# Performance work log

Measured on AMD Instinct MI355X. Metric: run time of the kernel, lower is better.

Reference implementation:

```python
import jax, jax.numpy as jnp
import numpy as np

B, S, D, H, HID = 64, 1024, 128, 4, 512
HD = D // H  # head dim = 32
EPS = 1e-5


def layer_norm(x, gamma, beta):
    mu = jnp.mean(x, axis=-1, keepdims=True)
    var = jnp.mean(jnp.square(x - mu), axis=-1, keepdims=True)
    return (x - mu) * jax.lax.rsqrt(var + EPS) * gamma + beta


def setup_inputs() -> dict:
    key = jax.random.key(0)
    ks = jax.random.split(key, 16)
    w = lambda k, shp: (jax.random.normal(k, shp, dtype=jnp.float32) * 0.02)
    return {
        "seq": jax.random.normal(ks[0], (B, S, D), dtype=jnp.float32),
        "mask": jnp.ones((B, S, 1), dtype=jnp.float32),
        "Wq": w(ks[1], (D, D)), "bq": jnp.zeros((D,), jnp.float32),
        "Wk": w(ks[2], (D, D)), "bk": jnp.zeros((D,), jnp.float32),
        "Wv": w(ks[3], (D, D)), "bv": jnp.zeros((D,), jnp.float32),
        "g1": jnp.ones((D,), jnp.float32), "be1": jnp.zeros((D,), jnp.float32),
        "g2": jnp.ones((D,), jnp.float32), "be2": jnp.zeros((D,), jnp.float32),
        "W1": w(ks[4], (D, HID)), "bm1": jnp.zeros((HID,), jnp.float32),
        "W2": w(ks[5], (HID, D)), "bm2": jnp.zeros((D,), jnp.float32),
    }


def reference(seq, mask, Wq, bq, Wk, bk, Wv, bv, g1, be1, g2, be2, W1, bm1, W2, bm2):
    # pre-norm queries; keys/values come from the RAW seq (SASRec quirk)
    q_in = layer_norm(seq, g1, be1)           # [B,S,D]
    keys = seq

    Q = (q_in @ Wq + bq).reshape(B, S, H, HD)
    K = (keys @ Wk + bk).reshape(B, S, H, HD)
    V = (keys @ Wv + bv).reshape(B, S, H, HD)

    scores = jnp.einsum("bqhd,bkhd->bhqk", Q, K) / jnp.sqrt(jnp.float32(HD))

    # key padding mask from sign of abs-sum over feature dim
    key_mask = jnp.sign(jnp.sum(jnp.abs(keys), axis=-1))      # [B,S]
    scores = jnp.where(key_mask[:, None, None, :] == 0, -jnp.inf, scores)

    # causal mask
    causal = jnp.tril(jnp.ones((S, S), dtype=bool))
    scores = jnp.where(causal[None, None], scores, -jnp.inf)

    w = jax.nn.softmax(scores, axis=-1)
    w = jnp.nan_to_num(w, nan=0.0, posinf=0.0, neginf=0.0)

    # query padding mask (on the NORMALIZED queries)
    query_mask = jnp.sign(jnp.sum(jnp.abs(q_in), axis=-1))    # [B,S]
    w = w * query_mask[:, None, :, None]
    attentions = w                                            # [B,H,S,S]

    attn_out = jnp.einsum("bhqk,bkhd->bqhd", w, V).reshape(B, S, D)

    x = attn_out + q_in
    x = layer_norm(x, g2, be2)
    h = jax.nn.relu(x @ W1 + bm1)
    y = h @ W2 + bm2 + x
    y = y * mask
    return y, attentions
```

## Files before the change

### kernel.cpp

```cpp
#include <hip/hip_runtime.h>
#include <cstddef>
#include <cstdint>

#define BB 64
#define SS 1024
#define DDIM 128
#define NH 4
#define HDIM 32
#define HIDD 512
#define EPSF 1e-5f
#define SCALEF 0.17677669529663687f

typedef __attribute__((ext_vector_type(8))) short short8;
typedef __attribute__((ext_vector_type(4))) short short4_t;
typedef __attribute__((ext_vector_type(4))) float f32x4;
typedef unsigned short ushort_t;

__device__ __forceinline__ unsigned short f2bf(float f) {
  unsigned u = __builtin_bit_cast(unsigned, f);
  unsigned r = (u + 0x7FFFu + ((u >> 16) & 1u)) >> 16;
  return (unsigned short)r;
}
__device__ __forceinline__ float bf2f(ushort_t h) {
  unsigned u = ((unsigned)h) << 16;
  return __builtin_bit_cast(float, u);
}

__global__ __launch_bounds__(256) void k_cvtw(
    const float* __restrict__ Wq, const float* __restrict__ Wk,
    const float* __restrict__ Wv, const float* __restrict__ W1,
    const float* __restrict__ W2,
    ushort_t* __restrict__ WqT, ushort_t* __restrict__ WkT,
    ushort_t* __restrict__ WvT, ushort_t* __restrict__ W1T,
    ushort_t* __restrict__ W2T) {
  __shared__ float tile[32][33];
  const int bid = blockIdx.x;
  const float* src; ushort_t* dst; int K, N, t0;
  if (bid < 16)       { src = Wq; dst = WqT; K = 128; N = 128; t0 = bid; }
  else if (bid < 32)  { src = Wk; dst = WkT; K = 128; N = 128; t0 = bid - 16; }
  else if (bid < 48)  { src = Wv; dst = WvT; K = 128; N = 128; t0 = bid - 32; }
  else if (bid < 112) { src = W1; dst = W1T; K = 128; N = 512; t0 = bid - 48; }
  else                { src = W2; dst = W2T; K = 512; N = 128; t0 = bid - 112; }
  const int ntile = N >> 5;
  const int k0 = (t0 / ntile) * 32, n0 = (t0 % ntile) * 32;
  const int t = threadIdx.x;
  const int r = t >> 3, c = (t & 7) * 4;
  float4 v = *(const float4*)(src + (size_t)(k0 + r) * N + n0 + c);
  tile[r][c] = v.x; tile[r][c + 1] = v.y; tile[r][c + 2] = v.z; tile[r][c + 3] = v.w;
  __syncthreads();
  ushort4 o;
  o.x = f2bf(tile[c + 0][r]); o.y = f2bf(tile[c + 1][r]);
  o.z = f2bf(tile[c + 2][r]); o.w = f2bf(tile[c + 3][r]);
  *(ushort4*)(dst + (size_t)(n0 + r) * K + k0 + c) = o;
}

__global__ __launch_bounds__(128) void k_ln1(const float* __restrict__ seq,
    const float* __restrict__ g1, const float* __restrict__ be1,
    ushort_t* __restrict__ q_in16, ushort_t* __restrict__ seq16,
    float* __restrict__ qmask, float* __restrict__ kmask) {
  int row = blockIdx.x, t = threadIdx.x;
  float v = seq[(size_t)row * DDIM + t];
  float s = v, a = fabsf(v);
  #pragma unroll
  for (int o = 32; o; o >>= 1) { s += __shfl_down(s, o); a += __shfl_down(a, o); }
  __shared__ float sm[4], sm2[2], sm3[2];
  if ((t & 63) == 0) { sm[t >> 6] = s; sm[2 + (t >> 6)] = a; }
  __syncthreads();
  float mean = (sm[0] + sm[1]) * (1.f / DDIM);
  float asum = sm[2] + sm[3];
  float d = v - mean;
  float sq = d * d;
  #pragma unroll
  for (int o = 32; o; o >>= 1) sq += __shfl_down(sq, o);
  if ((t & 63) == 0) sm2[t >> 6] = sq;
  __syncthreads();
  float var = (sm2[0] + sm2[1]) * (1.f / DDIM);
  float qv = d * rsqrtf(var + EPSF) * g1[t] + be1[t];
  q_in16[(size_t)row * DDIM + t] = f2bf(qv);
  seq16[(size_t)row * DDIM + t] = f2bf(v);
  float aq = fabsf(qv);
  #pragma unroll
  for (int o = 32; o; o >>= 1) aq += __shfl_down(aq, o);
  if ((t & 63) == 0) sm3[t >> 6] = aq;
  __syncthreads();
  if (t == 0) {
    kmask[row] = asum > 0.f ? 1.f : 0.f;
    qmask[row] = (sm3[0] + sm3[1]) > 0.f ? 1.f : 0.f;
  }
}

__global__ __launch_bounds__(256) void k_qkv_mfma(
    const ushort_t* __restrict__ q_in16, const ushort_t* __restrict__ seq16,
    const ushort_t* __restrict__ WqT, const ushort_t* __restrict__ WkT,
    const ushort_t* __restrict__ WvT,
    const float* __restrict__ bq, const float* __restrict__ bk,
    const float* __restrict__ bv,
    ushort_t* __restrict__ Qo, ushort_t* __restrict__ Ko,
    ushort_t* __restrict__ Vo) {
  const int m = blockIdx.y;
  const ushort_t* A = (m == 0) ? q_in16 : seq16;
  const ushort_t* WT = (m == 0) ? WqT : (m == 1 ? WkT : WvT);
  const float* bias = (m == 0) ? bq : (m == 1 ? bk : bv);
  ushort_t* O = (m == 0) ? Qo : (m == 1 ? Ko : Vo);
  const float sc = (m == 0) ? SCALEF : 1.0f;
  const int t = threadIdx.x, w = t >> 6, lane = t & 63;
  const int lr = lane & 15, lg = lane >> 4;
  const int row = blockIdx.x * 64 + w * 16;

  short8 a[4];
  #pragma unroll
  for (int s = 0; s < 4; ++s)
    a[s] = *(const short8*)(A + (size_t)(row + lr) * DDIM + s * 32 + lg * 8);

  #pragma unroll
  for (int nt = 0; nt < 8; ++nt) {
    f32x4 acc = {0.f, 0.f, 0.f, 0.f};
    #pragma unroll
    for (int s = 0; s < 4; ++s) {
      short8 b = *(const short8*)(WT + (size_t)(nt * 16 + lr) * DDIM + s * 32 + lg * 8);
      acc = __builtin_amdgcn_mfma_f32_16x16x32_bf16(b, a[s], acc, 0, 0, 0);
    }
    const int n0 = nt * 16 + lg * 4;
    const float4 bb4 = *(const float4*)(bias + n0);
    short4_t o4;
    o4[0] = (short)f2bf((acc[0] + bb4.x) * sc);
    o4[1] = (short)f2bf((acc[1] + bb4.y) * sc);
    o4[2] = (short)f2bf((acc[2] + bb4.z) * sc);
    o4[3] = (short)f2bf((acc[3] + bb4.w) * sc);
    *(short4_t*)(O + (size_t)(row + lr) * DDIM + n0) = o4;
  }
}

__global__ __launch_bounds__(256) void k_attn_mfma(
    const ushort_t* __restrict__ Q, const ushort_t* __restrict__ K,
    const ushort_t* __restrict__ V,
    const float* __restrict__ qmask, const float* __restrict__ kmask,
    float* __restrict__ attn, float* __restrict__ xo) {
  __shared__ __align__(16) ushort_t Ks[64 * 40];
  __shared__ __align__(16) ushort_t Vts[32 * 72];
  __shared__ __align__(16) ushort_t Wb[4][16 * 88];

  const int t = threadIdx.x;
  const int w = t >> 6, lane = t & 63, lr = lane & 15, lg = lane >> 4;
  const int qi = 15 - (int)blockIdx.x;
  const int q0 = qi << 6;
  const int h = blockIdx.y, b = blockIdx.z;
  const int kend = q0 + 64;
  const int nch = kend >> 6;

  const size_t bS = (size_t)b * SS;
  const ushort_t* Qh = Q + bS * DDIM + h * HDIM;
  const ushort_t* Kh = K + bS * DDIM + h * HDIM;
  const ushort_t* Vh = V + bS * DDIM + h * HDIM;
  float* attn_bh = attn + (size_t)(b * NH + h) * ((size_t)SS * SS);

  {
    const int cnt4 = (SS - kend) >> 2;
    for (int r = w; r < 64; r += 4) {
      float* rowp = attn_bh + (size_t)(q0 + r) * SS + kend;
      for (int c = lane; c < cnt4; c += 64)
        *(f32x4*)(rowp + (size_t)c * 4) = (f32x4){0.f, 0.f, 0.f, 0.f};
    }
  }

  const int qrow = q0 + w * 16 + lr;
  const short8 qf = *(const short8*)(Qh + (size_t)qrow * DDIM + lg * 8);

  const int skr = t >> 2, skc = (t & 3) * 8;

  float lsum = 0.f;
  short8 kreg = *(const short8*)(Kh + (size_t)skr * DDIM + skc);

  for (int c = 0; c < nch; ++c) {
    const int kc = c << 6;
    __syncthreads();
    *(short8*)(Ks + skr * 40 + skc) = kreg;
    if (c + 1 < nch)
      kreg = *(const short8*)(Kh + (size_t)(kc + 64 + skr) * DDIM + skc);
    __syncthreads();
    short8 kf[4];
    #pragma unroll
    for (int T = 0; T < 4; ++T)
      kf[T] = *(const short8*)(Ks + (T * 16 + lr) * 40 + lg * 8);
    f32x4 acc[4];
    #pragma unroll
    for (int T = 0; T < 4; ++T)
      acc[T] = __builtin_amdgcn_mfma_f32_16x16x32_bf16(kf[T], qf,
                                                       (f32x4){0.f, 0.f, 0.f, 0.f}, 0, 0, 0);
    #pragma unroll
    for (int T = 0; T < 4; ++T) {
      const int k0 = kc + T * 16 + lg * 4;
      const float4 km4 = *(const float4*)(kmask + bS + k0);
      #pragma unroll
      for (int r = 0; r < 4; ++r) {
        const float kmv = r == 0 ? km4.x : (r == 1 ? km4.y : (r == 2 ? km4.z : km4.w));
        const bool dead = (kmv == 0.f) || (k0 + r > qrow);
        lsum += dead ? 0.f : __expf(acc[T][r]);
      }
    }
  }
  float ssum = lsum;
  ssum += __shfl_xor(ssum, 16);
  ssum += __shfl_xor(ssum, 32);
  const float qm = qmask[bS + qrow];
  const float inv = (ssum > 0.f) ? qm / ssum : 0.f;

  ushort_t* myW = &Wb[w][0];
  f32x4 o0 = {0.f, 0.f, 0.f, 0.f}, o1 = {0.f, 0.f, 0.f, 0.f};

  short8 kreg2 = *(const short8*)(Kh + (size_t)skr * DDIM + skc);
  short8 vreg  = *(const short8*)(Vh + (size_t)lane * DDIM + w * 8);

  for (int c = 0; c < nch; ++c) {
    const int kc = c << 6;
    __syncthreads();
    *(short8*)(Ks + skr * 40 + skc) = kreg2;
    #pragma unroll
    for (int j = 0; j < 8; ++j) Vts[(w * 8 + j) * 72 + lane] = (ushort_t)vreg[j];
    if (c + 1 < nch) {
      kreg2 = *(const short8*)(Kh + (size_t)(kc + 64 + skr) * DDIM + skc);
      vreg  = *(const short8*)(Vh + (size_t)(kc + 64 + lane) * DDIM + w * 8);
    }
    __syncthreads();
    short8 kf[4];
    #pragma unroll
    for (int T = 0; T < 4; ++T)
      kf[T] = *(const short8*)(Ks + (T * 16 + lr) * 40 + lg * 8);
    f32x4 acc[4];
    #pragma unroll
    for (int T = 0; T < 4; ++T)
      acc[T] = __builtin_amdgcn_mfma_f32_16x16x32_bf16(kf[T], qf,
                                                       (f32x4){0.f, 0.f, 0.f, 0.f}, 0, 0, 0);
    #pragma unroll
    for (int T = 0; T < 4; ++T) {
      const int k0 = kc + T * 16 + lg * 4;
      const float4 km4 = *(const float4*)(kmask + bS + k0);
      f32x4 wv4;
      #pragma unroll
      for (int r = 0; r < 4; ++r) {
        const float kmv = r == 0 ? km4.x : (r == 1 ? km4.y : (r == 2 ? km4.z : km4.w));
        const bool dead = (kmv == 0.f) || (k0 + r > qrow);
        wv4[r] = dead ? 0.f : __expf(acc[T][r]) * inv;
      }
      *(f32x4*)(attn_bh + (size_t)qrow * SS + k0) = wv4;
      short4_t p4;
      p4[0] = (short)f2bf(wv4[0]); p4[1] = (short)f2bf(wv4[1]);
      p4[2] = (short)f2bf(wv4[2]); p4[3] = (short)f2bf(wv4[3]);
      *(short4_t*)(myW + lr * 88 + T * 16 + lg * 4) = p4;
    }
    const short8 af0 = *(const short8*)(myW + lr * 88 + lg * 8);
    const short8 af1 = *(const short8*)(myW + lr * 88 + 32 + lg * 8);
    const short8 vb00 = *(const short8*)(Vts + (size_t)(lr) * 72 + lg * 8);
    const short8 vb10 = *(const short8*)(Vts + (size_t)(lr) * 72 + 32 + lg * 8);
    const short8 vb01 = *(const short8*)(Vts + (size_t)(16 + lr) * 72 + lg * 8);
    const short8 vb11 = *(const short8*)(Vts + (size_t)(16 + lr) * 72 + 32 + lg * 8);
    o0 = __builtin_amdgcn_mfma_f32_16x16x32_bf16(vb00, af0, o0, 0, 0, 0);
    o0 = __builtin_amdgcn_mfma_f32_16x16x32_bf16(vb10, af1, o0, 0, 0, 0);
    o1 = __builtin_amdgcn_mfma_f32_16x16x32_bf16(vb01, af0, o1, 0, 0, 0);
    o1 = __builtin_amdgcn_mfma_f32_16x16x32_bf16(vb11, af1, o1, 0, 0, 0);
  }

  {
    float* op = xo + (bS + qrow) * DDIM + h * HDIM;
    *(f32x4*)(op + lg * 4) = o0;
    *(f32x4*)(op + 16 + lg * 4) = o1;
  }
}

__global__ __launch_bounds__(256) void k_mlp_fused(
    const float* __restrict__ xo, const ushort_t* __restrict__ q_in16,
    const float* __restrict__ g2, const float* __restrict__ be2,
    const ushort_t* __restrict__ W1T, const float* __restrict__ bm1,
    const ushort_t* __restrict__ W2T, const float* __restrict__ bm2,
    const float* __restrict__ mask, float* __restrict__ y) {
  __shared__ __align__(16) ushort_t xls[64 * 136];
  __shared__ __align__(16) ushort_t hs[4][16 * 140];
  const int t = threadIdx.x, w = t >> 6, lane = t & 63;
  const int lr = lane & 15, lg = lane >> 4;
  const int row0 = blockIdx.x * 64;

  {
    const int r = t >> 2, s = t & 3;
    const size_t base = (size_t)(row0 + r) * DDIM + s * 32;
    float v[32];
    float sum = 0.f, sq = 0.f;
    #pragma unroll
    for (int i = 0; i < 4; ++i) {
      const f32x4 x4a = *(const f32x4*)(xo + base + i * 8);
      const f32x4 x4b = *(const f32x4*)(xo + base + i * 8 + 4);
      const short8 q8 = *(const short8*)(q_in16 + base + i * 8);
      #pragma unroll
      for (int j = 0; j < 4; ++j) {
        v[i * 8 + j] = x4a[j] + bf2f((ushort_t)q8[j]);
        v[i * 8 + 4 + j] = x4b[j] + bf2f((ushort_t)q8[4 + j]);
      }
    }
    #pragma unroll
    for (int i = 0; i < 32; ++i) { sum += v[i]; sq += v[i] * v[i]; }
    sum += __shfl_xor(sum, 1); sum += __shfl_xor(sum, 2);
    sq  += __shfl_xor(sq, 1);  sq  += __shfl_xor(sq, 2);
    const float mean = sum * (1.f / DDIM);
    const float var = sq * (1.f / DDIM) - mean * mean;
    const float rsq = rsqrtf(var + EPSF);
    #pragma unroll
    for (int i = 0; i < 8; ++i) {
      const f32x4 g4 = *(const f32x4*)(g2 + s * 32 + i * 4);
      const f32x4 b4 = *(const f32x4*)(be2 + s * 32 + i * 4);
      short4_t o4;
      #pragma unroll
      for (int j = 0; j < 4; ++j)
        o4[j] = (short)f2bf((v[i * 4 + j] - mean) * rsq * g4[j] + b4[j]);
      *(short4_t*)(xls + r * 136 + s * 32 + i * 4) = o4;
    }
  }
  __syncthreads();

  ushort_t* myh = &hs[w][0];
  short8 xa[4];
  #pragma unroll
  for (int s = 0; s < 4; ++s)
    xa[s] = *(const short8*)(xls + (w * 16 + lr) * 136 + s * 32 + lg * 8);

  f32x4 yacc[8];
  #pragma unroll
  for (int i = 0; i < 8; ++i) yacc[i] = (f32x4){0.f, 0.f, 0.f, 0.f};

  for (int c = 0; c < 4; ++c) {
    #pragma unroll
    for (int nt = 0; nt < 8; ++nt) {
      f32x4 acc = {0.f, 0.f, 0.f, 0.f};
      #pragma unroll
      for (int s = 0; s < 4; ++s) {
        short8 b = *(const short8*)(W1T + (size_t)(c * 128 + nt * 16 + lr) * DDIM + s * 32 + lg * 8);
        acc = __builtin_amdgcn_mfma_f32_16x16x32_bf16(b, xa[s], acc, 0, 0, 0);
      }
      const int n0 = nt * 16 + lg * 4;
      const float4 bb4 = *(const float4*)(bm1 + c * 128 + n0);
      short4_t hp;
      hp[0] = (short)f2bf(fmaxf(acc[0] + bb4.x, 0.f));
      hp[1] = (short)f2bf(fmaxf(acc[1] + bb4.y, 0.f));
      hp[2] = (short)f2bf(fmaxf(acc[2] + bb4.z, 0.f));
      hp[3] = (short)f2bf(fmaxf(acc[3] + bb4.w, 0.f));
      *(short4_t*)(myh + lr * 140 + n0) = hp;
    }
    short8 a2[4];
    #pragma unroll
    for (int s = 0; s < 4; ++s)
      a2[s] = *(const short8*)(myh + lr * 140 + s * 32 + lg * 8);
    #pragma unroll
    for (int nt = 0; nt < 8; ++nt) {
      #pragma unroll
      for (int s = 0; s < 4; ++s) {
        short8 b = *(const short8*)(W2T + (size_t)(nt * 16 + lr) * HIDD + c * 128 + s * 32 + lg * 8);
        yacc[nt] = __builtin_amdgcn_mfma_f32_16x16x32_bf16(b, a2[s], yacc[nt], 0, 0, 0);
      }
    }
  }

  const int rr = row0 + w * 16 + lr;
  const float mk = mask[rr];
  #pragma unroll
  for (int nt = 0; nt < 8; ++nt) {
    const int n0 = nt * 16 + lg * 4;
    const float4 bb4 = *(const float4*)(bm2 + n0);
    const ushort4 xv = *(const ushort4*)(xls + (w * 16 + lr) * 136 + n0);
    f32x4 out;
    out[0] = (yacc[nt][0] + bb4.x + bf2f(xv.x)) * mk;
    out[1] = (yacc[nt][1] + bb4.y + bf2f(xv.y)) * mk;
    out[2] = (yacc[nt][2] + bb4.z + bf2f(xv.z)) * mk;
    out[3] = (yacc[nt][3] + bb4.w + bf2f(xv.w)) * mk;
    *(f32x4*)(y + (size_t)rr * DDIM + n0) = out;
  }
}

extern "C" void kernel_launch(void* const* d_in, const int* in_sizes, int n_in,
                              void* d_out, int out_size, void* d_ws, size_t ws_size,
                              hipStream_t stream) {
  const float* seq  = (const float*)d_in[0];
  const float* mask = (const float*)d_in[1];
  const float* Wq = (const float*)d_in[2];
  const float* bq = (const float*)d_in[3];
  const float* Wk = (const float*)d_in[4];
  const float* bk = (const float*)d_in[5];
  const float* Wv = (const float*)d_in[6];
  const float* bv = (const float*)d_in[7];
  const float* g1 = (const float*)d_in[8];
  const float* be1 = (const float*)d_in[9];
  const float* g2 = (const float*)d_in[10];
  const float* be2 = (const float*)d_in[11];
  const float* W1 = (const float*)d_in[12];
  const float* bm1 = (const float*)d_in[13];
  const float* W2 = (const float*)d_in[14];
  const float* bm2 = (const float*)d_in[15];

  float* ws   = (float*)d_ws;
  float* xb   = ws;
  float* qmk  = ws + 8388608;
  float* kmk  = ws + 8454144;
  ushort_t* sbase  = (ushort_t*)(ws + 8519680);
  ushort_t* Qb     = sbase;
  ushort_t* Kb     = sbase + 8388608;
  ushort_t* Vb     = sbase + 16777216;
  ushort_t* q_in16 = sbase + 25165824;
  ushort_t* seq16  = sbase + 33554432;
  ushort_t* WqT    = sbase + 41943040;
  ushort_t* WkT    = WqT + 16384;
  ushort_t* WvT    = WkT + 16384;
  ushort_t* W1T    = WvT + 16384;
  ushort_t* W2T    = W1T + 65536;

  float* y    = (float*)d_out;
  float* attn = y + 8388608;

  hipLaunchKernelGGL(k_cvtw, dim3(176), dim3(256), 0, stream,
                     Wq, Wk, Wv, W1, W2, WqT, WkT, WvT, W1T, W2T);
  hipLaunchKernelGGL(k_ln1, dim3(BB * SS), dim3(128), 0, stream,
                     seq, g1, be1, q_in16, seq16, qmk, kmk);
  hipLaunchKernelGGL(k_qkv_mfma, dim3(1024, 3), dim3(256), 0, stream,
                     q_in16, seq16, WqT, WkT, WvT, bq, bk, bv, Qb, Kb, Vb);
  hipLaunchKernelGGL(k_attn_mfma, dim3(16, NH, BB), dim3(256), 0, stream,
                     Qb, Kb, Vb, qmk, kmk, attn, xb);
  hipLaunchKernelGGL(k_mlp_fused, dim3(1024), dim3(256), 0, stream,
                     xb, q_in16, g2, be2, W1T, bm1, W2T, bm2, mask, y);
}
```

Baseline: 672.8 us.

## Double-buffer attention K/V smem, use exp2 softmax, fuse K/V projection, vectorize LN1

The attention kernel now double-buffers its K and V shared-memory tiles, so each chunk needs one barrier instead of two and the next tile's global load overlaps compute. Q is pre-scaled by log2(e) so the softmax can use exp2f, and the attention-matrix writes become nontemporal stores. The QKV kernel computes K and V together from a single load of seq, which drops one grid slice. LayerNorm1 now handles 8 rows per block with float4 loads and warp-only reductions. Together these target barrier stalls, redundant input reads and cache pollution from the large attention output.

```diff
diff --git a/kernel.cpp b/kernel.cpp
--- a/kernel.cpp
+++ b/kernel.cpp
@@ -10,6 +10,7 @@
 #define HIDD 512
 #define EPSF 1e-5f
 #define SCALEF 0.17677669529663687f
+#define LOG2E 1.4426950408889634f
 
 typedef __attribute__((ext_vector_type(8))) short short8;
 typedef __attribute__((ext_vector_type(4))) short short4_t;
@@ -54,38 +55,43 @@
   *(ushort4*)(dst + (size_t)(n0 + r) * K + k0 + c) = o;
 }
 
-__global__ __launch_bounds__(128) void k_ln1(const float* __restrict__ seq,
+__global__ __launch_bounds__(256) void k_ln1(const float* __restrict__ seq,
     const float* __restrict__ g1, const float* __restrict__ be1,
     ushort_t* __restrict__ q_in16, ushort_t* __restrict__ seq16,
     float* __restrict__ qmask, float* __restrict__ kmask) {
-  int row = blockIdx.x, t = threadIdx.x;
-  float v = seq[(size_t)row * DDIM + t];
-  float s = v, a = fabsf(v);
-  #pragma unroll
-  for (int o = 32; o; o >>= 1) { s += __shfl_down(s, o); a += __shfl_down(a, o); }
-  __shared__ float sm[4], sm2[2], sm3[2];
-  if ((t & 63) == 0) { sm[t >> 6] = s; sm[2 + (t >> 6)] = a; }
-  __syncthreads();
-  float mean = (sm[0] + sm[1]) * (1.f / DDIM);
-  float asum = sm[2] + sm[3];
-  float d = v - mean;
-  float sq = d * d;
-  #pragma unroll
-  for (int o = 32; o; o >>= 1) sq += __shfl_down(sq, o);
-  if ((t & 63) == 0) sm2[t >> 6] = sq;
-  __syncthreads();
-  float var = (sm2[0] + sm2[1]) * (1.f / DDIM);
-  float qv = d * rsqrtf(var + EPSF) * g1[t] + be1[t];
-  q_in16[(size_t)row * DDIM + t] = f2bf(qv);
-  seq16[(size_t)row * DDIM + t] = f2bf(v);
-  float aq = fabsf(qv);
-  #pragma unroll
-  for (int o = 32; o; o >>= 1) aq += __shfl_down(aq, o);
-  if ((t & 63) == 0) sm3[t >> 6] = aq;
-  __syncthreads();
-  if (t == 0) {
+  const int t = threadIdx.x;
+  const int r = t >> 5, cl = (t & 31) * 4;
+  const int row = blockIdx.x * 8 + r;
+  const size_t base = (size_t)row * DDIM + cl;
+  const f32x4 v4 = *(const f32x4*)(seq + base);
+  float sum = v4[0] + v4[1] + v4[2] + v4[3];
+  float asum = fabsf(v4[0]) + fabsf(v4[1]) + fabsf(v4[2]) + fabsf(v4[3]);
+  #pragma unroll
+  for (int o = 1; o < 32; o <<= 1) { sum += __shfl_xor(sum, o); asum += __shfl_xor(asum, o); }
+  const float mean = sum * (1.f / DDIM);
+  f32x4 d;
+  #pragma unroll
+  for (int j = 0; j < 4; ++j) d[j] = v4[j] - mean;
+  float sq = d[0] * d[0] + d[1] * d[1] + d[2] * d[2] + d[3] * d[3];
+  #pragma unroll
+  for (int o = 1; o < 32; o <<= 1) sq += __shfl_xor(sq, o);
+  const float rsq = rsqrtf(sq * (1.f / DDIM) + EPSF);
+  const float4 g4 = *(const float4*)(g1 + cl);
+  const float4 b4 = *(const float4*)(be1 + cl);
+  float qv[4];
+  qv[0] = d[0] * rsq * g4.x + b4.x; qv[1] = d[1] * rsq * g4.y + b4.y;
+  qv[2] = d[2] * rsq * g4.z + b4.z; qv[3] = d[3] * rsq * g4.w + b4.w;
+  short4_t q4, s4;
+  #pragma unroll
+  for (int j = 0; j < 4; ++j) { q4[j] = (short)f2bf(qv[j]); s4[j] = (short)f2bf(v4[j]); }
+  *(short4_t*)(q_in16 + base) = q4;
+  *(short4_t*)(seq16 + base) = s4;
+  float aq = fabsf(qv[0]) + fabsf(qv[1]) + fabsf(qv[2]) + fabsf(qv[3]);
+  #pragma unroll
+  for (int o = 1; o < 32; o <<= 1) aq += __shfl_xor(aq, o);
+  if ((t & 31) == 0) {
     kmask[row] = asum > 0.f ? 1.f : 0.f;
-    qmask[row] = (sm3[0] + sm3[1]) > 0.f ? 1.f : 0.f;
+    qmask[row] = aq > 0.f ? 1.f : 0.f;
   }
 }
 
@@ -98,36 +104,59 @@
     ushort_t* __restrict__ Qo, ushort_t* __restrict__ Ko,
     ushort_t* __restrict__ Vo) {
   const int m = blockIdx.y;
-  const ushort_t* A = (m == 0) ? q_in16 : seq16;
-  const ushort_t* WT = (m == 0) ? WqT : (m == 1 ? WkT : WvT);
-  const float* bias = (m == 0) ? bq : (m == 1 ? bk : bv);
-  ushort_t* O = (m == 0) ? Qo : (m == 1 ? Ko : Vo);
-  const float sc = (m == 0) ? SCALEF : 1.0f;
   const int t = threadIdx.x, w = t >> 6, lane = t & 63;
   const int lr = lane & 15, lg = lane >> 4;
   const int row = blockIdx.x * 64 + w * 16;
 
-  short8 a[4];
-  #pragma unroll
-  for (int s = 0; s < 4; ++s)
-    a[s] = *(const short8*)(A + (size_t)(row + lr) * DDIM + s * 32 + lg * 8);
-
-  #pragma unroll
-  for (int nt = 0; nt < 8; ++nt) {
-    f32x4 acc = {0.f, 0.f, 0.f, 0.f};
-    #pragma unroll
-    for (int s = 0; s < 4; ++s) {
-      short8 b = *(const short8*)(WT + (size_t)(nt * 16 + lr) * DDIM + s * 32 + lg * 8);
-      acc = __builtin_amdgcn_mfma_f32_16x16x32_bf16(b, a[s], acc, 0, 0, 0);
-    }
-    const int n0 = nt * 16 + lg * 4;
-    const float4 bb4 = *(const float4*)(bias + n0);
-    short4_t o4;
-    o4[0] = (short)f2bf((acc[0] + bb4.x) * sc);
-    o4[1] = (short)f2bf((acc[1] + bb4.y) * sc);
-    o4[2] = (short)f2bf((acc[2] + bb4.z) * sc);
-    o4[3] = (short)f2bf((acc[3] + bb4.w) * sc);
-    *(short4_t*)(O + (size_t)(row + lr) * DDIM + n0) = o4;
+  if (m == 0) {
+    const float sc = SCALEF * LOG2E;
+    short8 a[4];
+    #pragma unroll
+    for (int s = 0; s < 4; ++s)
+      a[s] = *(const short8*)(q_in16 + (size_t)(row + lr) * DDIM + s * 32 + lg * 8);
+    #pragma unroll
+    for (int nt = 0; nt < 8; ++nt) {
+      f32x4 acc = {0.f, 0.f, 0.f, 0.f};
+      #pragma unroll
+      for (int s = 0; s < 4; ++s) {
+        short8 b = *(const short8*)(WqT + (size_t)(nt * 16 + lr) * DDIM + s * 32 + lg * 8);
+        acc = __builtin_amdgcn_mfma_f32_16x16x32_bf16(b, a[s], acc, 0, 0, 0);
+      }
+      const int n0 = nt * 16 + lg * 4;
+      const float4 bb4 = *(const float4*)(bq + n0);
+      short4_t o4;
+      o4[0] = (short)f2bf((acc[0] + bb4.x) * sc);
+      o4[1] = (short)f2bf((acc[1] + bb4.y) * sc);
+      o4[2] = (short)f2bf((acc[2] + bb4.z) * sc);
+      o4[3] = (short)f2bf((acc[3] + bb4.w) * sc);
+      *(short4_t*)(Qo + (size_t)(row + lr) * DDIM + n0) = o4;
+    }
+  } else {
+    short8 a[4];
+    #pragma unroll
+    for (int s = 0; s < 4; ++s)
+      a[s] = *(const short8*)(seq16 + (size_t)(row + lr) * DDIM + s * 32 + lg * 8);
+    #pragma unroll
+    for (int nt = 0; nt < 8; ++nt) {
+      f32x4 accK = {0.f, 0.f, 0.f, 0.f}, accV = {0.f, 0.f, 0.f, 0.f};
+      #pragma unroll
+      for (int s = 0; s < 4; ++s) {
+        short8 bk8 = *(const short8*)(WkT + (size_t)(nt * 16 + lr) * DDIM + s * 32 + lg * 8);
+        short8 bv8 = *(const short8*)(WvT + (size_t)(nt * 16 + lr) * DDIM + s * 32 + lg * 8);
+        accK = __builtin_amdgcn_mfma_f32_16x16x32_bf16(bk8, a[s], accK, 0, 0, 0);
+        accV = __builtin_amdgcn_mfma_f32_16x16x32_bf16(bv8, a[s], accV, 0, 0, 0);
+      }
+      const int n0 = nt * 16 + lg * 4;
+      const float4 bk4 = *(const float4*)(bk + n0);
+      const float4 bv4 = *(const float4*)(bv + n0);
+      short4_t k4, v4;
+      k4[0] = (short)f2bf(accK[0] + bk4.x); v4[0] = (short)f2bf(accV[0] + bv4.x);
+      k4[1] = (short)f2bf(accK[1] + bk4.y); v4[1] = (short)f2bf(accV[1] + bv4.y);
+      k4[2] = (short)f2bf(accK[2] + bk4.z); v4[2] = (short)f2bf(accV[2] + bv4.z);
+      k4[3] = (short)f2bf(accK[3] + bk4.w); v4[3] = (short)f2bf(accV[3] + bv4.w);
+      *(short4_t*)(Ko + (size_t)(row + lr) * DDIM + n0) = k4;
+      *(short4_t*)(Vo + (size_t)(row + lr) * DDIM + n0) = v4;
+    }
   }
 }
 
@@ -136,8 +165,8 @@
     const ushort_t* __restrict__ V,
     const float* __restrict__ qmask, const float* __restrict__ kmask,
     float* __restrict__ attn, float* __restrict__ xo) {
-  __shared__ __align__(16) ushort_t Ks[64 * 40];
-  __shared__ __align__(16) ushort_t Vts[32 * 72];
+  __shared__ __align__(16) ushort_t Ks[2][64 * 40];
+  __shared__ __align__(16) ushort_t Vts[2][32 * 72];
   __shared__ __align__(16) ushort_t Wb[4][16 * 88];
 
   const int t = threadIdx.x;
@@ -156,10 +185,11 @@
 
   {
     const int cnt4 = (SS - kend) >> 2;
+    const f32x4 z = {0.f, 0.f, 0.f, 0.f};
     for (int r = w; r < 64; r += 4) {
       float* rowp = attn_bh + (size_t)(q0 + r) * SS + kend;
       for (int c = lane; c < cnt4; c += 64)
-        *(f32x4*)(rowp + (size_t)c * 4) = (f32x4){0.f, 0.f, 0.f, 0.f};
+        __builtin_nontemporal_store(z, (f32x4*)(rowp + (size_t)c * 4));
     }
   }
 
@@ -169,34 +199,38 @@
   const int skr = t >> 2, skc = (t & 3) * 8;
 
   float lsum = 0.f;
-  short8 kreg = *(const short8*)(Kh + (size_t)skr * DDIM + skc);
-
-  for (int c = 0; c < nch; ++c) {
-    const int kc = c << 6;
+  {
+    short8 kreg = *(const short8*)(Kh + (size_t)skr * DDIM + skc);
+    *(short8*)(Ks[0] + skr * 40 + skc) = kreg;
     __syncthreads();
-    *(short8*)(Ks + skr * 40 + skc) = kreg;
-    if (c + 1 < nch)
-      kreg = *(const short8*)(Kh + (size_t)(kc + 64 + skr) * DDIM + skc);
-    __syncthreads();
-    short8 kf[4];
-    #pragma unroll
-    for (int T = 0; T < 4; ++T)
-      kf[T] = *(const short8*)(Ks + (T * 16 + lr) * 40 + lg * 8);
-    f32x4 acc[4];
-    #pragma unroll
-    for (int T = 0; T < 4; ++T)
-      acc[T] = __builtin_amdgcn_mfma_f32_16x16x32_bf16(kf[T], qf,
-                                                       (f32x4){0.f, 0.f, 0.f, 0.f}, 0, 0, 0);
-    #pragma unroll
-    for (int T = 0; T < 4; ++T) {
-      const int k0 = kc + T * 16 + lg * 4;
-      const float4 km4 = *(const float4*)(kmask + bS + k0);
-      #pragma unroll
-      for (int r = 0; r < 4; ++r) {
-        const float kmv = r == 0 ? km4.x : (r == 1 ? km4.y : (r == 2 ? km4.z : km4.w));
-        const bool dead = (kmv == 0.f) || (k0 + r > qrow);
-        lsum += dead ? 0.f : __expf(acc[T][r]);
-      }
+    for (int c = 0; c < nch; ++c) {
+      const int kc = c << 6;
+      const int cur = c & 1;
+      if (c + 1 < nch)
+        kreg = *(const short8*)(Kh + (size_t)(kc + 64 + skr) * DDIM + skc);
+      short8 kf[4];
+      #pragma unroll
+      for (int T = 0; T < 4; ++T)
+        kf[T] = *(const short8*)(Ks[cur] + (T * 16 + lr) * 40 + lg * 8);
+      f32x4 acc[4];
+      #pragma unroll
+      for (int T = 0; T < 4; ++T)
+        acc[T] = __builtin_amdgcn_mfma_f32_16x16x32_bf16(kf[T], qf,
+                                                         (f32x4){0.f, 0.f, 0.f, 0.f}, 0, 0, 0);
+      #pragma unroll
+      for (int T = 0; T < 4; ++T) {
+        const int k0 = kc + T * 16 + lg * 4;
+        const float4 km4 = *(const float4*)(kmask + bS + k0);
+        #pragma unroll
+        for (int r = 0; r < 4; ++r) {
+          const float kmv = r == 0 ? km4.x : (r == 1 ? km4.y : (r == 2 ? km4.z : km4.w));
+          const bool dead = (kmv == 0.f) || (k0 + r > qrow);
+          lsum += dead ? 0.f : exp2f(acc[T][r]);
+        }
+      }
+      if (c + 1 < nch)
+        *(short8*)(Ks[cur ^ 1] + skr * 40 + skc) = kreg;
+      __syncthreads();
     }
   }
   float ssum = lsum;
@@ -208,56 +242,63 @@
   ushort_t* myW = &Wb[w][0];
   f32x4 o0 = {0.f, 0.f, 0.f, 0.f}, o1 = {0.f, 0.f, 0.f, 0.f};
 
-  short8 kreg2 = *(const short8*)(Kh + (size_t)skr * DDIM + skc);
-  short8 vreg  = *(const short8*)(Vh + (size_t)lane * DDIM + w * 8);
-
-  for (int c = 0; c < nch; ++c) {
-    const int kc = c << 6;
+  {
+    short8 kreg = *(const short8*)(Kh + (size_t)skr * DDIM + skc);
+    short8 vreg = *(const short8*)(Vh + (size_t)lane * DDIM + w * 8);
+    *(short8*)(Ks[0] + skr * 40 + skc) = kreg;
+    #pragma unroll
+    for (int j = 0; j < 8; ++j) Vts[0][(w * 8 + j) * 72 + lane] = (ushort_t)vreg[j];
     __syncthreads();
-    *(short8*)(Ks + skr * 40 + skc) = kreg2;
-    #pragma unroll
-    for (int j = 0; j < 8; ++j) Vts[(w * 8 + j) * 72 + lane] = (ushort_t)vreg[j];
-    if (c + 1 < nch) {
-      kreg2 = *(const short8*)(Kh + (size_t)(kc + 64 + skr) * DDIM + skc);
-      vreg  = *(const short8*)(Vh + (size_t)(kc + 64 + lane) * DDIM + w * 8);
-    }
-    __syncthreads();
-    short8 kf[4];
-    #pragma unroll
-    for (int T = 0; T < 4; ++T)
-      kf[T] = *(const short8*)(Ks + (T * 16 + lr) * 40 + lg * 8);
-    f32x4 acc[4];
-    #pragma unroll
-    for (int T = 0; T < 4; ++T)
-      acc[T] = __builtin_amdgcn_mfma_f32_16x16x32_bf16(kf[T], qf,
-                                                       (f32x4){0.f, 0.f, 0.f, 0.f}, 0, 0, 0);
-    #pragma unroll
-    for (int T = 0; T < 4; ++T) {
-      const int k0 = kc + T * 16 + lg * 4;
-      const float4 km4 = *(const float4*)(kmask + bS + k0);
-      f32x4 wv4;
-      #pragma unroll
-      for (int r = 0; r < 4; ++r) {
-        const float kmv = r == 0 ? km4.x : (r == 1 ? km4.y : (r == 2 ? km4.z : km4.w));
-        const bool dead = (kmv == 0.f) || (k0 + r > qrow);
-        wv4[r] = dead ? 0.f : __expf(acc[T][r]) * inv;
-      }
-      *(f32x4*)(attn_bh + (size_t)qrow * SS + k0) = wv4;
-      short4_t p4;
-      p4[0] = (short)f2bf(wv4[0]); p4[1] = (short)f2bf(wv4[1]);
-      p4[2] = (short)f2bf(wv4[2]); p4[3] = (short)f2bf(wv4[3]);
-      *(short4_t*)(myW + lr * 88 + T * 16 + lg * 4) = p4;
-    }
-    const short8 af0 = *(const short8*)(myW + lr * 88 + lg * 8);
-    const short8 af1 = *(const short8*)(myW + lr * 88 + 32 + lg * 8);
-    const short8 vb00 = *(const short8*)(Vts + (size_t)(lr) * 72 + lg * 8);
-    const short8 vb10 = *(const short8*)(Vts + (size_t)(lr) * 72 + 32 + lg * 8);
-    const short8 vb01 = *(const short8*)(Vts + (size_t)(16 + lr) * 72 + lg * 8);
-    const short8 vb11 = *(const short8*)(Vts + (size_t)(16 + lr) * 72 + 32 + lg * 8);
-    o0 = __builtin_amdgcn_mfma_f32_16x16x32_bf16(vb00, af0, o0, 0, 0, 0);
-    o0 = __builtin_amdgcn_mfma_f32_16x16x32_bf16(vb10, af1, o0, 0, 0, 0);
-    o1 = __builtin_amdgcn_mfma_f32_16x16x32_bf16(vb01, af0, o1, 0, 0, 0);
-    o1 = __builtin_amdgcn_mfma_f32_16x16x32_bf16(vb11, af1, o1, 0, 0, 0);
+    for (int c = 0; c < nch; ++c) {
+      const int kc = c << 6;
+      const int cur = c & 1;
+      if (c + 1 < nch) {
+        kreg = *(const short8*)(Kh + (size_t)(kc + 64 + skr) * DDIM + skc);
+        vreg = *(const short8*)(Vh + (size_t)(kc + 64 + lane) * DDIM + w * 8);
+      }
+      short8 kf[4];
+      #pragma unroll
+      for (int T = 0; T < 4; ++T)
+        kf[T] = *(const short8*)(Ks[cur] + (T * 16 + lr) * 40 + lg * 8);
+      f32x4 acc[4];
+      #pragma unroll
+      for (int T = 0; T < 4; ++T)
+        acc[T] = __builtin_amdgcn_mfma_f32_16x16x32_bf16(kf[T], qf,
+                                                         (f32x4){0.f, 0.f, 0.f, 0.f}, 0, 0, 0);
+      #pragma unroll
+      for (int T = 0; T < 4; ++T) {
+        const int k0 = kc + T * 16 + lg * 4;
+        const float4 km4 = *(const float4*)(kmask + bS + k0);
+        f32x4 wv4;
+        #pragma unroll
+        for (int r = 0; r < 4; ++r) {
+          const float kmv = r == 0 ? km4.x : (r == 1 ? km4.y : (r == 2 ? km4.z : km4.w));
+          const bool dead = (kmv == 0.f) || (k0 + r > qrow);
+          wv4[r] = dead ? 0.f : exp2f(acc[T][r]) * inv;
+        }
+        __builtin_nontemporal_store(wv4, (f32x4*)(attn_bh + (size_t)qrow * SS + k0));
+        short4_t p4;
+        p4[0] = (short)f2bf(wv4[0]); p4[1] = (short)f2bf(wv4[1]);
+        p4[2] = (short)f2bf(wv4[2]); p4[3] = (short)f2bf(wv4[3]);
+        *(short4_t*)(myW + lr * 88 + T * 16 + lg * 4) = p4;
+      }
+      const short8 af0 = *(const short8*)(myW + lr * 88 + lg * 8);
+      const short8 af1 = *(const short8*)(myW + lr * 88 + 32 + lg * 8);
+      const short8 vb00 = *(const short8*)(Vts[cur] + (size_t)(lr) * 72 + lg * 8);
+      const short8 vb10 = *(const short8*)(Vts[cur] + (size_t)(lr) * 72 + 32 + lg * 8);
+      const short8 vb01 = *(const short8*)(Vts[cur] + (size_t)(16 + lr) * 72 + lg * 8);
+      const short8 vb11 = *(const short8*)(Vts[cur] + (size_t)(16 + lr) * 72 + 32 + lg * 8);
+      o0 = __builtin_amdgcn_mfma_f32_16x16x32_bf16(vb00, af0, o0, 0, 0, 0);
+      o0 = __builtin_amdgcn_mfma_f32_16x16x32_bf16(vb10, af1, o0, 0, 0, 0);
+      o1 = __builtin_amdgcn_mfma_f32_16x16x32_bf16(vb01, af0, o1, 0, 0, 0);
+      o1 = __builtin_amdgcn_mfma_f32_16x16x32_bf16(vb11, af1, o1, 0, 0, 0);
+      if (c + 1 < nch) {
+        *(short8*)(Ks[cur ^ 1] + skr * 40 + skc) = kreg;
+        #pragma unroll
+        for (int j = 0; j < 8; ++j) Vts[cur ^ 1][(w * 8 + j) * 72 + lane] = (ushort_t)vreg[j];
+      }
+      __syncthreads();
+    }
   }
 
   {
@@ -414,9 +455,9 @@
 
   hipLaunchKernelGGL(k_cvtw, dim3(176), dim3(256), 0, stream,
                      Wq, Wk, Wv, W1, W2, WqT, WkT, WvT, W1T, W2T);
-  hipLaunchKernelGGL(k_ln1, dim3(BB * SS), dim3(128), 0, stream,
+  hipLaunchKernelGGL(k_ln1, dim3(BB * SS / 8), dim3(256), 0, stream,
                      seq, g1, be1, q_in16, seq16, qmk, kmk);
-  hipLaunchKernelGGL(k_qkv_mfma, dim3(1024, 3), dim3(256), 0, stream,
+  hipLaunchKernelGGL(k_qkv_mfma, dim3(1024, 2), dim3(256), 0, stream,
                      q_in16, seq16, WqT, WkT, WvT, bq, bk, bv, Qb, Kb, Vb);
   hipLaunchKernelGGL(k_attn_mfma, dim3(16, NH, BB), dim3(256), 0, stream,
                      Qb, Kb, Vb, qmk, kmk, attn, xb);
```

Measured after the change: 573.7 us. 14.7% less time.
